# Performance work log

Measured on AMD Instinct MI355X. Metric: run time of the kernel, lower is better.

## Reference

```python
import jax, jax.numpy as jnp
import numpy as np

B, T, EMB, H = 8, 1024, 128, 8


def setup_inputs() -> dict:
    key = jax.random.key(0)
    ks = jax.random.split(key, 7)
    s = 0.02
    return {
        "x": jax.random.normal(ks[0], (B, T, EMB), dtype=jnp.float32),
        "mask": jax.random.randint(ks[1], (1, T, T), 0, 2, dtype=jnp.int32),
        "Wk": (jax.random.normal(ks[2], (EMB * H, EMB), dtype=jnp.float32) * s),
        "Wq": (jax.random.normal(ks[3], (EMB * H, EMB), dtype=jnp.float32) * s),
        "Wv": (jax.random.normal(ks[4], (EMB * H, EMB), dtype=jnp.float32) * s),
        "Wu": (jax.random.normal(ks[5], (EMB, EMB * H), dtype=jnp.float32) * s),
        "bu": (jax.random.normal(ks[6], (EMB,), dtype=jnp.float32) * s),
    }


def reference(x, mask, Wk, Wq, Wv, Wu, bu):
    b, t, e = x.shape  # e == emb; per-head dim also == emb in this module
    h = Wk.shape[0] // e
    # projections: (b,t,e) @ (e, h*e) -> (b,t,h,e) -> (b,h,t,e)
    q = (x @ Wq.T).reshape(b, t, h, e).transpose(0, 2, 1, 3)
    k = (x @ Wk.T).reshape(b, t, h, e).transpose(0, 2, 1, 3)
    v = (x @ Wv.T).reshape(b, t, h, e).transpose(0, 2, 1, 3)
    scale = e ** 0.25  # torch scales q and k each by e**(1/4)
    dot = jnp.einsum('bhqe,bhke->bhqk', q / scale, k / scale)
    # causal mask: strictly-upper triangle (offset=1) set to -inf FIRST
    causal = jnp.triu(jnp.ones((t, t), dtype=bool), k=1)
    dot = jnp.where(causal, -jnp.inf, dot)
    # padding mask: where mask==0 set to -1e9 (overwrites -inf where overlapping)
    dot = jnp.where(mask[:, None] == 0, jnp.float32(-1e9), dot)
    attn = jax.nn.softmax(dot, axis=-1)
    out = jnp.einsum('bhqk,bhke->bhqe', attn, v)
    out = out.transpose(0, 2, 1, 3).reshape(b, t, h * e)
    return out @ Wu.T + bu
```

## Files before the change

### kernel.cpp

```cpp
#include <hip/hip_runtime.h>

#define Bn 8
#define Hn 8
#define Tn 1024
#define Dn 128

typedef __attribute__((ext_vector_type(8))) short bf16x8;
typedef __attribute__((ext_vector_type(4))) float f32x4;

typedef __attribute__((address_space(3))) unsigned int lds_as_t;
typedef __attribute__((address_space(1))) const unsigned int glb_as_t;

static __device__ __forceinline__ void gload_lds16(const unsigned short* g, unsigned short* l) {
    __builtin_amdgcn_global_load_lds((glb_as_t*)g, (lds_as_t*)l, 16, 0, 0);
}

static __device__ __forceinline__ unsigned short f2bf(float f) {
    union { float f; unsigned int u; } v; v.f = f;
    unsigned int u = v.u;
    return (unsigned short)((u + 0x7FFFu + ((u >> 16) & 1u)) >> 16);
}

__global__ __launch_bounds__(256) void prep_kernel(
    const float* __restrict__ x,  const float* __restrict__ Wq,
    const float* __restrict__ Wk, const float* __restrict__ Wv,
    const float* __restrict__ Wu, const int* __restrict__ mask,
    unsigned short* __restrict__ xb,  unsigned short* __restrict__ wqB,
    unsigned short* __restrict__ wkB, unsigned short* __restrict__ wvB,
    unsigned short* __restrict__ wuB, unsigned long long* __restrict__ bits)
{
    const int blk = blockIdx.x;
    const int tid = threadIdx.x;

    if (blk < 1408) {
        const float* in; unsigned short* out; int i4;
        if (blk < 1024)      { in = x;  out = xb;  i4 = blk * 256 + tid; }
        else if (blk < 1152) { in = Wq; out = wqB; i4 = (blk - 1024) * 256 + tid; }
        else if (blk < 1280) { in = Wk; out = wkB; i4 = (blk - 1152) * 256 + tid; }
        else                 { in = Wv; out = wvB; i4 = (blk - 1280) * 256 + tid; }
        float4 f = ((const float4*)in)[i4];
        ushort4 o;
        o.x = f2bf(f.x); o.y = f2bf(f.y); o.z = f2bf(f.z); o.w = f2bf(f.w);
        int base = i4 * 4;
        int row = base >> 7, col = base & 127;
        int scol = (((col >> 3) ^ (row & 15)) << 3) | (col & 7);
        *(ushort4*)(out + row * 128 + scol) = o;
    } else if (blk < 1536) {
        int i4 = (blk - 1408) * 256 + tid;
        float4 f = ((const float4*)Wu)[i4];
        ushort4 o;
        o.x = f2bf(f.x); o.y = f2bf(f.y); o.z = f2bf(f.z); o.w = f2bf(f.w);
        ((ushort4*)wuB)[i4] = o;
    } else {
        int wid  = (blk - 1536) * 4 + (tid >> 6);
        int lane = tid & 63;
#pragma unroll
        for (int i = 0; i < 4; i++) {
            int widx = wid * 4 + i;
            int row = widx >> 4, kt = widx & 15;
            int v = mask[row * Tn + kt * 64 + lane];
            unsigned long long b = __ballot(v != 0);
            if (lane == 0) bits[widx] = b;
        }
    }
}

__global__ __launch_bounds__(256, 2) void qkv_kernel(
    const unsigned short* __restrict__ xb,
    const unsigned short* __restrict__ wqB,
    const unsigned short* __restrict__ wkB,
    const unsigned short* __restrict__ wvB,
    unsigned short* __restrict__ Q,
    unsigned short* __restrict__ K,
    unsigned short* __restrict__ Vt)
{
    const int bx = blockIdx.x, by = blockIdx.y;
    const int wave = threadIdx.x >> 6;
    const int lane = threadIdx.x & 63;
    const int l16  = lane & 15;
    const int quad = lane >> 4;
    const int wm = wave & 1, wn = wave >> 1;

    __shared__ __align__(16) unsigned short As[128 * 128];
    __shared__ __align__(16) unsigned short Bs[128 * 128];

    const int which = by >> 3;
    const unsigned short* wsel = (which == 0) ? wqB : (which == 1) ? wkB : wvB;
    const unsigned short* Ag = xb + (size_t)bx * 128 * 128;
    const unsigned short* Bg = wsel + (size_t)(by & 7) * 128 * 128;

#pragma unroll
    for (int i = 0; i < 8; i++) {
        int base = (wave * 8 + i) * 512;
        gload_lds16(Ag + base + lane * 8, &As[base]);
        gload_lds16(Bg + base + lane * 8, &Bs[base]);
    }
    __syncthreads();

    bf16x8 a[4][4];
#pragma unroll
    for (int mt = 0; mt < 4; mt++) {
        int row = wm * 64 + mt * 16 + l16;
#pragma unroll
        for (int ks = 0; ks < 4; ks++)
            a[mt][ks] = *(const bf16x8*)(&As[row * 128 + (((ks * 4 + quad) ^ (row & 15)) << 3)]);
    }

    f32x4 acc[4][4];
#pragma unroll
    for (int nt = 0; nt < 4; nt++) {
        int row = wn * 64 + nt * 16 + l16;
        bf16x8 b4[4];
#pragma unroll
        for (int ks = 0; ks < 4; ks++)
            b4[ks] = *(const bf16x8*)(&Bs[row * 128 + (((ks * 4 + quad) ^ (row & 15)) << 3)]);
#pragma unroll
        for (int mt = 0; mt < 4; mt++) {
            f32x4 c = {0.f, 0.f, 0.f, 0.f};
#pragma unroll
            for (int ks = 0; ks < 4; ks++)
                c = __builtin_amdgcn_mfma_f32_16x16x32_bf16(a[mt][ks], b4[ks], c, 0, 0, 0);
            acc[mt][nt] = c;
        }
    }

    const int h_ = by & 7;
#pragma unroll
    for (int mt = 0; mt < 4; mt++) {
        int m_base = bx * 128 + wm * 64 + mt * 16 + quad * 4;
        int b_ = m_base >> 10;
        int t0 = m_base & 1023;
#pragma unroll
        for (int nt = 0; nt < 4; nt++) {
            int ncol = wn * 64 + nt * 16 + l16;
            if (which == 2) {
                int kt_ = t0 >> 6, tc0 = t0 & 63;
                int e_ = ncol;
                size_t off = ((((size_t)(b_ * Hn + h_) * 16 + kt_) * 128 + e_) << 6)
                           + ((((tc0 >> 3) ^ (e_ & 7)) << 3) | (tc0 & 7));
                ushort4 v4;
                v4.x = f2bf(acc[mt][nt][0]); v4.y = f2bf(acc[mt][nt][1]);
                v4.z = f2bf(acc[mt][nt][2]); v4.w = f2bf(acc[mt][nt][3]);
                *(ushort4*)(Vt + off) = v4;
            } else {
#pragma unroll
                for (int r = 0; r < 4; r++) {
                    int t_ = t0 + r;
                    unsigned short v = f2bf(acc[mt][nt][r]);
                    size_t rowoff = ((size_t)((b_ * Hn + h_) * Tn + t_)) * Dn;
                    if (which == 0) {
                        Q[rowoff + ncol] = v;
                    } else {
                        int nc = ((((ncol >> 3) ^ (t_ & 15)) << 3) | (ncol & 7));
                        K[rowoff + nc] = v;
                    }
                }
            }
        }
    }
}

__global__ __launch_bounds__(256, 2) void attn_kernel(
    const unsigned short* __restrict__ Q,
    const unsigned short* __restrict__ K,
    const unsigned short* __restrict__ Vt,
    const unsigned long long* __restrict__ mbits,
    unsigned short* __restrict__ AO)
{
    const int id   = blockIdx.x;
    const int qb   = (id & 7) ^ (7 * ((id >> 8) & 1));
    const int bh   = (id >> 3) & 63;
    const int wave = threadIdx.x >> 6;
    const int lane = threadIdx.x & 63;
    const int l16  = lane & 15;
    const int quad = lane >> 4;

    __shared__ __align__(16) unsigned short kbuf[2][64 * 128];
    __shared__ __align__(16) unsigned short vbuf[2][128 * 64];
    __shared__ __align__(16) unsigned short pbuf[4][16][72];

    const unsigned short* Qb = Q  + (size_t)bh * Tn * Dn;
    const unsigned short* Kb = K  + (size_t)bh * Tn * Dn;
    const unsigned short* Vb = Vt + (size_t)bh * (16 * 128 * 64);

    const int ktmax = 2 * qb + 1;
    const int q0 = qb * 128 + wave * 32;

    bf16x8 qf[2][4];
#pragma unroll
    for (int st = 0; st < 2; st++)
#pragma unroll
        for (int ks = 0; ks < 4; ks++)
            qf[st][ks] = *(const bf16x8*)(Qb + (size_t)(q0 + st * 16 + l16) * Dn + ks * 32 + quad * 8);

    bf16x8 ones;
#pragma unroll
    for (int j = 0; j < 8; j++) ones[j] = (short)0x3F80;

    f32x4 o[2][8];
#pragma unroll
    for (int st = 0; st < 2; st++)
#pragma unroll
        for (int et = 0; et < 8; et++) o[st][et] = (f32x4){0.f, 0.f, 0.f, 0.f};
    f32x4 lacc[2];
    lacc[0] = (f32x4){0.f, 0.f, 0.f, 0.f};
    lacc[1] = (f32x4){0.f, 0.f, 0.f, 0.f};

    const float SL = 0.12752041570284543f;

#pragma unroll
    for (int i = 0; i < 4; i++) {
        int base = (wave * 4 + i) * 512;
        gload_lds16(Kb + base + lane * 8, &kbuf[0][base]);
        gload_lds16(Vb + base + lane * 8, &vbuf[0][base]);
    }

    for (int kt = 0; kt <= ktmax; kt++) {
        const int cur = kt & 1;
        __syncthreads();

        if (kt < ktmax) {
            const unsigned short* Kg = Kb + (kt + 1) * (64 * 128);
            const unsigned short* Vg = Vb + (kt + 1) * (128 * 64);
#pragma unroll
            for (int i = 0; i < 4; i++) {
                int base = (wave * 4 + i) * 512;
                gload_lds16(Kg + base + lane * 8, &kbuf[cur ^ 1][base]);
                gload_lds16(Vg + base + lane * 8, &vbuf[cur ^ 1][base]);
            }
        }

        unsigned long long mw[2][4];
#pragma unroll
        for (int st = 0; st < 2; st++)
#pragma unroll
            for (int r = 0; r < 4; r++)
                mw[st][r] = mbits[(size_t)(q0 + st * 16 + quad * 4 + r) * 16 + kt];

        f32x4 s[2][4];
#pragma unroll
        for (int nt = 0; nt < 4; nt++) {
            bf16x8 b4[4];
#pragma unroll
            for (int ks = 0; ks < 4; ks++)
                b4[ks] = *(const bf16x8*)(&kbuf[cur][(nt * 16 + l16) * 128 + (((ks * 4 + quad) ^ l16) << 3)]);
#pragma unroll
            for (int st = 0; st < 2; st++) {
                f32x4 c = {0.f, 0.f, 0.f, 0.f};
#pragma unroll
                for (int ks = 0; ks < 4; ks++)
                    c = __builtin_amdgcn_mfma_f32_16x16x32_bf16(qf[st][ks], b4[ks], c, 0, 0, 0);
                s[st][nt] = c;
            }
        }

        const int kc0 = kt * 64;
        bf16x8 pf[2][2];
#pragma unroll
        for (int st = 0; st < 2; st++) {
#pragma unroll
            for (int nt = 0; nt < 4; nt++) {
                int bi = nt * 16 + l16;
                int key = kc0 + bi;
#pragma unroll
                for (int r = 0; r < 4; r++) {
                    int q = q0 + st * 16 + quad * 4 + r;
                    bool live = ((mw[st][r] >> bi) & 1ULL) && (key <= q);
                    float p = live ? __builtin_amdgcn_exp2f(s[st][nt][r] * SL) : 0.f;
                    pbuf[wave][quad * 4 + r][bi] = f2bf(p);
                }
            }
#pragma unroll
            for (int k2 = 0; k2 < 2; k2++)
                pf[st][k2] = *(const bf16x8*)(&pbuf[wave][l16][k2 * 32 + quad * 8]);
        }

#pragma unroll
        for (int st = 0; st < 2; st++)
#pragma unroll
            for (int k2 = 0; k2 < 2; k2++)
                lacc[st] = __builtin_amdgcn_mfma_f32_16x16x32_bf16(pf[st][k2], ones, lacc[st], 0, 0, 0);

#pragma unroll
        for (int et = 0; et < 8; et++) {
#pragma unroll
            for (int k2 = 0; k2 < 2; k2++) {
                bf16x8 b = *(const bf16x8*)(&vbuf[cur][(et * 16 + l16) * 64 + (((k2 * 4 + quad) ^ (l16 & 7)) << 3)]);
                o[0][et] = __builtin_amdgcn_mfma_f32_16x16x32_bf16(pf[0][k2], b, o[0][et], 0, 0, 0);
                o[1][et] = __builtin_amdgcn_mfma_f32_16x16x32_bf16(pf[1][k2], b, o[1][et], 0, 0, 0);
            }
        }
    }

    {
        bool deg = false;
#pragma unroll
        for (int st = 0; st < 2; st++)
#pragma unroll
            for (int r = 0; r < 4; r++) deg |= (lacc[st][r] == 0.f);
        if (__ballot(deg) != 0ULL) {
            unsigned short dsel[2][4];
#pragma unroll
            for (int st = 0; st < 2; st++)
#pragma unroll
                for (int r = 0; r < 4; r++)
                    dsel[st][r] = (lacc[st][r] == 0.f) ? (unsigned short)0x3F80 : (unsigned short)0;
            for (int kt = 0; kt < 16; kt++) {
                unsigned long long mw[2][4];
#pragma unroll
                for (int st = 0; st < 2; st++)
#pragma unroll
                    for (int r = 0; r < 4; r++)
                        mw[st][r] = mbits[(size_t)(q0 + st * 16 + quad * 4 + r) * 16 + kt];
                bf16x8 pf[2][2];
#pragma unroll
                for (int st = 0; st < 2; st++) {
#pragma unroll
                    for (int nt = 0; nt < 4; nt++) {
                        int bi = nt * 16 + l16;
#pragma unroll
                        for (int r = 0; r < 4; r++)
                            pbuf[wave][quad * 4 + r][bi] = ((mw[st][r] >> bi) & 1ULL) ? (unsigned short)0 : dsel[st][r];
                    }
#pragma unroll
                    for (int k2 = 0; k2 < 2; k2++)
                        pf[st][k2] = *(const bf16x8*)(&pbuf[wave][l16][k2 * 32 + quad * 8]);
                }
#pragma unroll
                for (int st = 0; st < 2; st++)
#pragma unroll
                    for (int k2 = 0; k2 < 2; k2++)
                        lacc[st] = __builtin_amdgcn_mfma_f32_16x16x32_bf16(pf[st][k2], ones, lacc[st], 0, 0, 0);
#pragma unroll
                for (int et = 0; et < 8; et++) {
#pragma unroll
                    for (int k2 = 0; k2 < 2; k2++) {
                        const unsigned short* vg = Vb + kt * (128 * 64)
                            + (et * 16 + l16) * 64 + (((k2 * 4 + quad) ^ (l16 & 7)) << 3);
                        bf16x8 b = *(const bf16x8*)vg;
                        o[0][et] = __builtin_amdgcn_mfma_f32_16x16x32_bf16(pf[0][k2], b, o[0][et], 0, 0, 0);
                        o[1][et] = __builtin_amdgcn_mfma_f32_16x16x32_bf16(pf[1][k2], b, o[1][et], 0, 0, 0);
                    }
                }
            }
        }
    }

    const int b_ = bh >> 3, h_ = bh & 7;
#pragma unroll
    for (int st = 0; st < 2; st++)
#pragma unroll
        for (int r = 0; r < 4; r++) {
            float inv = 1.f / lacc[st][r];
            int q = q0 + st * 16 + quad * 4 + r;
            size_t rowoff = (size_t)(b_ * Tn + q) * (Hn * Dn) + h_ * Dn;
#pragma unroll
            for (int et = 0; et < 8; et++)
                AO[rowoff + et * 16 + l16] = f2bf(o[st][et][r] * inv);
        }
}

__global__ __launch_bounds__(256) void outproj_kernel(
    const unsigned short* __restrict__ AO,
    const unsigned short* __restrict__ wuB,
    const float* __restrict__ bu,
    float* __restrict__ out)
{
    const int wave = threadIdx.x >> 6;
    const int lane = threadIdx.x & 63;
    const int l16  = lane & 15;
    const int quad = lane >> 4;
    const int m0 = blockIdx.x * 16;

    __shared__ float red[4][16][128];

    f32x4 acc[8];
#pragma unroll
    for (int nt = 0; nt < 8; nt++) acc[nt] = (f32x4){0.f, 0.f, 0.f, 0.f};

    const int kk0 = wave * 8;
#pragma unroll
    for (int g = 0; g < 8; g++) {
        int kk = kk0 + g;
        bf16x8 a = *(const bf16x8*)(AO + (size_t)(m0 + l16) * 1024 + kk * 32 + quad * 8);
#pragma unroll
        for (int nt = 0; nt < 8; nt++) {
            bf16x8 b = *(const bf16x8*)(wuB + (size_t)(nt * 16 + l16) * 1024 + kk * 32 + quad * 8);
            acc[nt] = __builtin_amdgcn_mfma_f32_16x16x32_bf16(a, b, acc[nt], 0, 0, 0);
        }
    }

#pragma unroll
    for (int nt = 0; nt < 8; nt++)
#pragma unroll
        for (int r = 0; r < 4; r++)
            red[wave][quad * 4 + r][nt * 16 + l16] = acc[nt][r];
    __syncthreads();

#pragma unroll
    for (int i = 0; i < 2; i++) {
        int flat = threadIdx.x * 2 + i;
        int row = flat >> 5, c4 = (flat & 31) * 4;
        f32x4 v = *(const f32x4*)(&red[0][row][c4]);
#pragma unroll
        for (int w = 1; w < 4; w++) {
            f32x4 p = *(const f32x4*)(&red[w][row][c4]);
            v[0] += p[0]; v[1] += p[1]; v[2] += p[2]; v[3] += p[3];
        }
        float4 bb = *(const float4*)(bu + c4);
        v[0] += bb.x; v[1] += bb.y; v[2] += bb.z; v[3] += bb.w;
        *(f32x4*)(out + (size_t)(m0 + row) * Dn + c4) = v;
    }
}

extern "C" void kernel_launch(void* const* d_in, const int* in_sizes, int n_in,
                              void* d_out, int out_size, void* d_ws, size_t ws_size,
                              hipStream_t stream) {
    const float* x   = (const float*)d_in[0];
    const int* mask  = (const int*)d_in[1];
    const float* Wk  = (const float*)d_in[2];
    const float* Wq  = (const float*)d_in[3];
    const float* Wv  = (const float*)d_in[4];
    const float* Wu  = (const float*)d_in[5];
    const float* bu  = (const float*)d_in[6];
    float* out = (float*)d_out;

    char* ws = (char*)d_ws;
    unsigned short* xb  = (unsigned short*)ws; ws += (size_t)8192 * 128 * 2;
    unsigned short* wqB = (unsigned short*)ws; ws += (size_t)1024 * 128 * 2;
    unsigned short* wkB = (unsigned short*)ws; ws += (size_t)1024 * 128 * 2;
    unsigned short* wvB = (unsigned short*)ws; ws += (size_t)1024 * 128 * 2;
    unsigned short* wuB = (unsigned short*)ws; ws += (size_t)128 * 1024 * 2;
    unsigned short* Qw  = (unsigned short*)ws; ws += (size_t)64 * 1024 * 128 * 2;
    unsigned short* Kw  = (unsigned short*)ws; ws += (size_t)64 * 1024 * 128 * 2;
    unsigned short* Vtw = (unsigned short*)ws; ws += (size_t)64 * 1024 * 128 * 2;
    unsigned short* AOw = (unsigned short*)ws; ws += (size_t)8192 * 1024 * 2;
    unsigned long long* mb = (unsigned long long*)ws; ws += (size_t)1024 * 16 * 8;

    prep_kernel<<<dim3(2560), 256, 0, stream>>>(x, Wq, Wk, Wv, Wu, mask,
                                                xb, wqB, wkB, wvB, wuB, mb);
    qkv_kernel<<<dim3(64, 24), 256, 0, stream>>>(xb, wqB, wkB, wvB, Qw, Kw, Vtw);
    attn_kernel<<<dim3(512), 256, 0, stream>>>(Qw, Kw, Vtw, mb, AOw);
    outproj_kernel<<<dim3(512), 256, 0, stream>>>(AOw, wuB, bu, out);
}
```

Baseline: 163.0 us.

## Pair causal query blocks per workgroup to balance attention work and share K/V tiles

The attention kernel now launches 256 workgroups of 512 threads instead of 512 of 256. Each workgroup handles query block a and its mirror 7-a for one batch-head, with each of the 8 waves owning 16 rows from each block. All workgroups therefore do the same causal work, and K/V tiles loaded into LDS serve both query blocks. The cost is one resident workgroup per CU, fewer workgroups overall, and waves sitting idle on the short block (alive0 false) during its later iterations.

```diff
diff --git a/kernel.cpp b/kernel.cpp
--- a/kernel.cpp
+++ b/kernel.cpp
@@ -160,16 +160,16 @@
     }
 }
 
-__global__ __launch_bounds__(256, 2) void attn_kernel(
+__global__ __launch_bounds__(512, 1) void attn_kernel(
     const unsigned short* __restrict__ Q,
     const unsigned short* __restrict__ K,
     const unsigned short* __restrict__ Vt,
     const unsigned long long* __restrict__ mbits,
     unsigned short* __restrict__ AO)
 {
-    const int id   = blockIdx.x;
-    const int qb   = (id & 7) ^ (7 * ((id >> 8) & 1));
-    const int bh   = (id >> 3) & 63;
+    const int blk  = blockIdx.x;
+    const int bh   = blk & 63;
+    const int a    = blk >> 6;
     const int wave = threadIdx.x >> 6;
     const int lane = threadIdx.x & 63;
     const int l16  = lane & 15;
@@ -177,21 +177,22 @@
 
     __shared__ __align__(16) unsigned short kbuf[2][64 * 128];
     __shared__ __align__(16) unsigned short vbuf[2][128 * 64];
-    __shared__ __align__(16) unsigned short pbuf[4][16][72];
+    __shared__ __align__(16) unsigned short pbuf[8][16][72];
 
     const unsigned short* Qb = Q  + (size_t)bh * Tn * Dn;
     const unsigned short* Kb = K  + (size_t)bh * Tn * Dn;
     const unsigned short* Vb = Vt + (size_t)bh * (16 * 128 * 64);
 
-    const int ktmax = 2 * qb + 1;
-    const int q0 = qb * 128 + wave * 32;
+    const int ktmax0   = 2 * a + 1;
+    const int blkktmax = 15 - 2 * a;
+    const int q0s[2] = { a * 128 + wave * 16, (7 - a) * 128 + wave * 16 };
 
     bf16x8 qf[2][4];
 #pragma unroll
     for (int st = 0; st < 2; st++)
 #pragma unroll
         for (int ks = 0; ks < 4; ks++)
-            qf[st][ks] = *(const bf16x8*)(Qb + (size_t)(q0 + st * 16 + l16) * Dn + ks * 32 + quad * 8);
+            qf[st][ks] = *(const bf16x8*)(Qb + (size_t)(q0s[st] + l16) * Dn + ks * 32 + quad * 8);
 
     bf16x8 ones;
 #pragma unroll
@@ -210,32 +211,39 @@
 
 #pragma unroll
     for (int i = 0; i < 4; i++) {
-        int base = (wave * 4 + i) * 512;
-        gload_lds16(Kb + base + lane * 8, &kbuf[0][base]);
-        gload_lds16(Vb + base + lane * 8, &vbuf[0][base]);
-    }
-
-    for (int kt = 0; kt <= ktmax; kt++) {
+        int idx = wave * 4 + i;
+        int base = (idx & 15) * 512;
+        if (idx < 16) gload_lds16(Kb + base + lane * 8, &kbuf[0][base]);
+        else          gload_lds16(Vb + base + lane * 8, &vbuf[0][base]);
+    }
+
+    for (int kt = 0; kt <= blkktmax; kt++) {
         const int cur = kt & 1;
         __syncthreads();
 
-        if (kt < ktmax) {
+        if (kt < blkktmax) {
             const unsigned short* Kg = Kb + (kt + 1) * (64 * 128);
             const unsigned short* Vg = Vb + (kt + 1) * (128 * 64);
 #pragma unroll
             for (int i = 0; i < 4; i++) {
-                int base = (wave * 4 + i) * 512;
-                gload_lds16(Kg + base + lane * 8, &kbuf[cur ^ 1][base]);
-                gload_lds16(Vg + base + lane * 8, &vbuf[cur ^ 1][base]);
-            }
-        }
+                int idx = wave * 4 + i;
+                int base = (idx & 15) * 512;
+                if (idx < 16) gload_lds16(Kg + base + lane * 8, &kbuf[cur ^ 1][base]);
+                else          gload_lds16(Vg + base + lane * 8, &vbuf[cur ^ 1][base]);
+            }
+        }
+
+        const bool alive0 = (kt <= ktmax0);
 
         unsigned long long mw[2][4];
 #pragma unroll
-        for (int st = 0; st < 2; st++)
+        for (int r = 0; r < 4; r++)
+            mw[1][r] = mbits[(size_t)(q0s[1] + quad * 4 + r) * 16 + kt];
+        if (alive0) {
 #pragma unroll
             for (int r = 0; r < 4; r++)
-                mw[st][r] = mbits[(size_t)(q0 + st * 16 + quad * 4 + r) * 16 + kt];
+                mw[0][r] = mbits[(size_t)(q0s[0] + quad * 4 + r) * 16 + kt];
+        }
 
         f32x4 s[2][4];
 #pragma unroll
@@ -244,50 +252,76 @@
 #pragma unroll
             for (int ks = 0; ks < 4; ks++)
                 b4[ks] = *(const bf16x8*)(&kbuf[cur][(nt * 16 + l16) * 128 + (((ks * 4 + quad) ^ l16) << 3)]);
-#pragma unroll
-            for (int st = 0; st < 2; st++) {
+            {
                 f32x4 c = {0.f, 0.f, 0.f, 0.f};
 #pragma unroll
                 for (int ks = 0; ks < 4; ks++)
-                    c = __builtin_amdgcn_mfma_f32_16x16x32_bf16(qf[st][ks], b4[ks], c, 0, 0, 0);
-                s[st][nt] = c;
+                    c = __builtin_amdgcn_mfma_f32_16x16x32_bf16(qf[1][ks], b4[ks], c, 0, 0, 0);
+                s[1][nt] = c;
+            }
+            if (alive0) {
+                f32x4 c = {0.f, 0.f, 0.f, 0.f};
+#pragma unroll
+                for (int ks = 0; ks < 4; ks++)
+                    c = __builtin_amdgcn_mfma_f32_16x16x32_bf16(qf[0][ks], b4[ks], c, 0, 0, 0);
+                s[0][nt] = c;
             }
         }
 
         const int kc0 = kt * 64;
         bf16x8 pf[2][2];
-#pragma unroll
-        for (int st = 0; st < 2; st++) {
+        {
 #pragma unroll
             for (int nt = 0; nt < 4; nt++) {
                 int bi = nt * 16 + l16;
                 int key = kc0 + bi;
 #pragma unroll
                 for (int r = 0; r < 4; r++) {
-                    int q = q0 + st * 16 + quad * 4 + r;
-                    bool live = ((mw[st][r] >> bi) & 1ULL) && (key <= q);
-                    float p = live ? __builtin_amdgcn_exp2f(s[st][nt][r] * SL) : 0.f;
+                    int q = q0s[1] + quad * 4 + r;
+                    bool live = ((mw[1][r] >> bi) & 1ULL) && (key <= q);
+                    float p = live ? __builtin_amdgcn_exp2f(s[1][nt][r] * SL) : 0.f;
                     pbuf[wave][quad * 4 + r][bi] = f2bf(p);
                 }
             }
 #pragma unroll
             for (int k2 = 0; k2 < 2; k2++)
-                pf[st][k2] = *(const bf16x8*)(&pbuf[wave][l16][k2 * 32 + quad * 8]);
-        }
-
-#pragma unroll
-        for (int st = 0; st < 2; st++)
+                pf[1][k2] = *(const bf16x8*)(&pbuf[wave][l16][k2 * 32 + quad * 8]);
+        }
+        if (alive0) {
+#pragma unroll
+            for (int nt = 0; nt < 4; nt++) {
+                int bi = nt * 16 + l16;
+                int key = kc0 + bi;
+#pragma unroll
+                for (int r = 0; r < 4; r++) {
+                    int q = q0s[0] + quad * 4 + r;
+                    bool live = ((mw[0][r] >> bi) & 1ULL) && (key <= q);
+                    float p = live ? __builtin_amdgcn_exp2f(s[0][nt][r] * SL) : 0.f;
+                    pbuf[wave][quad * 4 + r][bi] = f2bf(p);
+                }
+            }
 #pragma unroll
             for (int k2 = 0; k2 < 2; k2++)
-                lacc[st] = __builtin_amdgcn_mfma_f32_16x16x32_bf16(pf[st][k2], ones, lacc[st], 0, 0, 0);
+                pf[0][k2] = *(const bf16x8*)(&pbuf[wave][l16][k2 * 32 + quad * 8]);
+        }
+
+#pragma unroll
+        for (int k2 = 0; k2 < 2; k2++)
+            lacc[1] = __builtin_amdgcn_mfma_f32_16x16x32_bf16(pf[1][k2], ones, lacc[1], 0, 0, 0);
+        if (alive0) {
+#pragma unroll
+            for (int k2 = 0; k2 < 2; k2++)
+                lacc[0] = __builtin_amdgcn_mfma_f32_16x16x32_bf16(pf[0][k2], ones, lacc[0], 0, 0, 0);
+        }
 
 #pragma unroll
         for (int et = 0; et < 8; et++) {
 #pragma unroll
             for (int k2 = 0; k2 < 2; k2++) {
                 bf16x8 b = *(const bf16x8*)(&vbuf[cur][(et * 16 + l16) * 64 + (((k2 * 4 + quad) ^ (l16 & 7)) << 3)]);
-                o[0][et] = __builtin_amdgcn_mfma_f32_16x16x32_bf16(pf[0][k2], b, o[0][et], 0, 0, 0);
                 o[1][et] = __builtin_amdgcn_mfma_f32_16x16x32_bf16(pf[1][k2], b, o[1][et], 0, 0, 0);
+                if (alive0)
+                    o[0][et] = __builtin_amdgcn_mfma_f32_16x16x32_bf16(pf[0][k2], b, o[0][et], 0, 0, 0);
             }
         }
     }
@@ -311,7 +345,7 @@
                 for (int st = 0; st < 2; st++)
 #pragma unroll
                     for (int r = 0; r < 4; r++)
-                        mw[st][r] = mbits[(size_t)(q0 + st * 16 + quad * 4 + r) * 16 + kt];
+                        mw[st][r] = mbits[(size_t)(q0s[st] + quad * 4 + r) * 16 + kt];
                 bf16x8 pf[2][2];
 #pragma unroll
                 for (int st = 0; st < 2; st++) {
@@ -352,7 +386,7 @@
 #pragma unroll
         for (int r = 0; r < 4; r++) {
             float inv = 1.f / lacc[st][r];
-            int q = q0 + st * 16 + quad * 4 + r;
+            int q = q0s[st] + quad * 4 + r;
             size_t rowoff = (size_t)(b_ * Tn + q) * (Hn * Dn) + h_ * Dn;
 #pragma unroll
             for (int et = 0; et < 8; et++)
@@ -440,6 +474,6 @@
     prep_kernel<<<dim3(2560), 256, 0, stream>>>(x, Wq, Wk, Wv, Wu, mask,
                                                 xb, wqB, wkB, wvB, wuB, mb);
     qkv_kernel<<<dim3(64, 24), 256, 0, stream>>>(xb, wqB, wkB, wvB, Qw, Kw, Vtw);
-    attn_kernel<<<dim3(512), 256, 0, stream>>>(Qw, Kw, Vtw, mb, AOw);
+    attn_kernel<<<dim3(256), 512, 0, stream>>>(Qw, Kw, Vtw, mb, AOw);
     outproj_kernel<<<dim3(512), 256, 0, stream>>>(AOw, wuB, bu, out);
 }
```

New measurement: 201.5 us. 23.6% more time.
